# Kernel tuning notes

Hardware: AMD Instinct MI355X
Metric: run time of the kernel (lower is better)

The kernel has to match this reference:

```python
import jax, jax.numpy as jnp
import numpy as np

V, BLK, D, H, L = 50257, 2048, 768, 12, 4
HD = D // H
EPS = 1e-5


def _ln(x, w, b):
    mu = jnp.mean(x, axis=-1, keepdims=True)
    var = jnp.mean(jnp.square(x - mu), axis=-1, keepdims=True)
    return (x - mu) * jax.lax.rsqrt(var + EPS) * w + b


def setup_inputs() -> dict:
    key = jax.random.key(0)
    ks = iter(jax.random.split(key, 32))
    s = 0.02
    idx = jax.random.randint(next(ks), (2, 2048), 0, V)
    inp = {
        "idx": idx,
        "wte": jax.random.normal(next(ks), (V, D), jnp.float32) * s,
        "wpe": jax.random.normal(next(ks), (BLK, D), jnp.float32) * s,
        # stacked per-layer params [L, ...]
        "ln1_w": jnp.ones((L, D), jnp.float32),
        "ln1_b": jnp.zeros((L, D), jnp.float32),
        "attn_w": jax.random.normal(next(ks), (L, D, 3 * D), jnp.float32) * s,
        "attn_b": jnp.zeros((L, 3 * D), jnp.float32),
        "proj_w": jax.random.normal(next(ks), (L, D, D), jnp.float32) * (s / np.sqrt(2 * L)),
        "proj_b": jnp.zeros((L, D), jnp.float32),
        "ln2_w": jnp.ones((L, D), jnp.float32),
        "ln2_b": jnp.zeros((L, D), jnp.float32),
        "fc_w": jax.random.normal(next(ks), (L, D, 4 * D), jnp.float32) * s,
        "fc_b": jnp.zeros((L, 4 * D), jnp.float32),
        "fcp_w": jax.random.normal(next(ks), (L, 4 * D, D), jnp.float32) * (s / np.sqrt(2 * L)),
        "fcp_b": jnp.zeros((L, D), jnp.float32),
        "lnf_w": jnp.ones((D,), jnp.float32),
        "lnf_b": jnp.zeros((D,), jnp.float32),
    }
    return inp


def _gpt_forward(idx, wte, wpe, ln1_w, ln1_b, attn_w, attn_b, proj_w, proj_b,
                 ln2_w, ln2_b, fc_w, fc_b, fcp_w, fcp_b, lnf_w, lnf_b):
    B, T = idx.shape
    x = wte[idx] + wpe[:T]  # [B,T,D]; dropout p=0 -> identity
    causal = jnp.tril(jnp.ones((T, T), bool))
    scale = 1.0 / np.sqrt(HD)

    def block(x, p):
        l1w, l1b, aw, ab, pw, pb, l2w, l2b, fw, fb, fpw, fpb = p
        h = _ln(x, l1w, l1b)
        qkv = h @ aw + ab  # [B,T,3D]
        q, k, v = jnp.split(qkv, 3, axis=-1)
        q = q.reshape(B, T, H, HD).transpose(0, 2, 1, 3)  # [B,H,T,hd]
        k = k.reshape(B, T, H, HD).transpose(0, 2, 1, 3)
        v = v.reshape(B, T, H, HD).transpose(0, 2, 1, 3)
        att = jnp.einsum('bhqd,bhkd->bhqk', q, k) * scale
        att = jnp.where(causal, att, -jnp.inf)
        att = jax.nn.softmax(att, axis=-1)
        y = jnp.einsum('bhqk,bhkd->bhqd', att, v)
        y = y.transpose(0, 2, 1, 3).reshape(B, T, D)
        x = x + y @ pw + pb
        h2 = _ln(x, l2w, l2b)
        m = jax.nn.gelu(h2 @ fw + fb, approximate=False) @ fpw + fpb
        return x + m, None

    params = (ln1_w, ln1_b, attn_w, attn_b, proj_w, proj_b,
              ln2_w, ln2_b, fc_w, fc_b, fcp_w, fcp_b)
    x, _ = jax.lax.scan(block, x, params)
    x = _ln(x, lnf_w, lnf_b)
    # inference path: logits only for last position, lm_head tied to wte
    logits = x[:, -1:, :] @ wte.T  # [B,1,V]
    return logits


def reference(idx, wte, wpe, ln1_w, ln1_b, attn_w, attn_b, proj_w, proj_b,
              ln2_w, ln2_b, fc_w, fc_b, fcp_w, fcp_b, lnf_w, lnf_b):
    return _gpt_forward(idx, wte, wpe, ln1_w, ln1_b, attn_w, attn_b, proj_w, proj_b,
                        ln2_w, ln2_b, fc_w, fc_b, fcp_w, fcp_b, lnf_w, lnf_b)
```

## Files before the change

kernel.cpp:

```cpp
#include <hip/hip_runtime.h>
#include <math.h>

#define V 50257
#define B 2
#define T 2048
#define D 768
#define H 12
#define HD 64
#define L 4
#define D3 (3*D)
#define D4 (4*D)
#define NTOK (B*T)
#define EPS 1e-5f

typedef __bf16 v8bf __attribute__((ext_vector_type(8)));
typedef __bf16 v4bf __attribute__((ext_vector_type(4)));
typedef unsigned short v8us __attribute__((ext_vector_type(8)));
typedef float  v4f  __attribute__((ext_vector_type(4)));

#define GAS(p) ((const __attribute__((address_space(1))) void*)(p))
#define LAS(p) ((__attribute__((address_space(3))) void*)(p))

#define LIDX(row, chunk) ((row)*64 + ((((chunk) ^ ((row)&7)))<<3))

__global__ __launch_bounds__(256) void embed_kernel(const int* __restrict__ idx,
                                                    const float* __restrict__ wte,
                                                    const float* __restrict__ wpe,
                                                    float* __restrict__ x) {
    int i = blockIdx.x * 256 + threadIdx.x;
    if (i >= NTOK * D) return;
    int pos = i / D;
    int d   = i - pos * D;
    int t   = pos & (T - 1);
    int tok = idx[pos];
    x[i] = wte[tok * D + d] + wpe[t * D + d];
}

__global__ __launch_bounds__(256) void ln_kernel(const float* __restrict__ X,
                                                 const float* __restrict__ w,
                                                 const float* __restrict__ b,
                                                 __bf16* __restrict__ Y,
                                                 int src_mul, int src_off) {
    int srow = blockIdx.x * src_mul + src_off;
    const float* xr = X + (size_t)srow * D;
    float v[3];
    float s = 0.f, s2 = 0.f;
    #pragma unroll
    for (int j = 0; j < 3; ++j) {
        v[j] = xr[threadIdx.x + 256 * j];
        s += v[j];
        s2 += v[j] * v[j];
    }
    #pragma unroll
    for (int off = 32; off; off >>= 1) {
        s  += __shfl_xor(s, off);
        s2 += __shfl_xor(s2, off);
    }
    __shared__ float ss[4], ss2[4];
    int wave = threadIdx.x >> 6, lane = threadIdx.x & 63;
    if (lane == 0) { ss[wave] = s; ss2[wave] = s2; }
    __syncthreads();
    s  = ss[0] + ss[1] + ss[2] + ss[3];
    s2 = ss2[0] + ss2[1] + ss2[2] + ss2[3];
    float mu  = s * (1.f / D);
    float var = s2 * (1.f / D) - mu * mu;
    float rs  = rsqrtf(var + EPS);
    __bf16* yr = Y + (size_t)blockIdx.x * D;
    #pragma unroll
    for (int j = 0; j < 3; ++j) {
        int c = threadIdx.x + 256 * j;
        yr[c] = (__bf16)((v[j] - mu) * rs * w[c] + b[c]);
    }
}

__global__ __launch_bounds__(256) void convw4_kernel(
        const float* __restrict__ aw_all,  const float* __restrict__ pw_all,
        const float* __restrict__ fw_all,  const float* __restrict__ fpw_all,
        __bf16* __restrict__ awt_all, __bf16* __restrict__ pwt_all,
        __bf16* __restrict__ fwt_all, __bf16* __restrict__ fpwt_all) {
    int bid = blockIdx.x;
    const int l = bid / 6912; bid -= l * 6912;
    const float* W; __bf16* Wt; int K, N, bx, by;
    if (bid < 1728)      {             W = aw_all  + (size_t)l * D  * D3; Wt = awt_all  + (size_t)l * D3 * D;  K = D;  N = D3; bx = bid % 72; by = bid / 72; }
    else if (bid < 2304) { bid -= 1728; W = pw_all  + (size_t)l * D  * D;  Wt = pwt_all  + (size_t)l * D  * D;  K = D;  N = D;  bx = bid % 24; by = bid / 24; }
    else if (bid < 4608) { bid -= 2304; W = fw_all  + (size_t)l * D  * D4; Wt = fwt_all  + (size_t)l * D4 * D;  K = D;  N = D4; bx = bid % 96; by = bid / 96; }
    else                 { bid -= 4608; W = fpw_all + (size_t)l * D4 * D;  Wt = fpwt_all + (size_t)l * D  * D4; K = D4; N = D;  bx = bid % 24; by = bid / 24; }
    __shared__ float t[32][33];
    const int n0 = bx * 32, k0 = by * 32;
    const int tx = threadIdx.x & 31, ty = threadIdx.x >> 5;
    #pragma unroll
    for (int p = 0; p < 4; ++p)
        t[ty + 8 * p][tx] = W[(size_t)(k0 + ty + 8 * p) * N + n0 + tx];
    __syncthreads();
    #pragma unroll
    for (int p = 0; p < 4; ++p)
        Wt[(size_t)(n0 + ty + 8 * p) * K + k0 + tx] = (__bf16)t[tx][ty + 8 * p];
}

template<bool OUTBF16, bool DOGELU, bool DORES>
__global__ __launch_bounds__(256) void gemm_bt(const __bf16* __restrict__ A,
                                               const __bf16* __restrict__ Wt,
                                               const float* __restrict__ bias,
                                               const float* __restrict__ res,
                                               void* __restrict__ Cout,
                                               int N, int K) {
    __shared__ __align__(16) __bf16 As[4096];
    __shared__ __align__(16) __bf16 Bs[4096];
    const int tid  = threadIdx.x;
    const int w    = tid >> 6;
    const int lane = tid & 63;
    const int row0 = blockIdx.y * 128;
    const int col0 = blockIdx.x * 128;

    const int c0   = w * 64 + lane;
    const int srow = ((c0 >> 6) & 3) * 16 + (c0 & 15);
    const int sk   = ((c0 >> 4) & 3) * 8;
    const __bf16* gA0 = A  + (size_t)(row0 + srow) * K + sk;
    const __bf16* gA1 = gA0 + (size_t)64 * K;
    const __bf16* gB0 = Wt + (size_t)(col0 + srow) * K + sk;
    const __bf16* gB1 = gB0 + (size_t)64 * K;
    __bf16* lA0 = As + (size_t)c0 * 8;
    __bf16* lA1 = As + (size_t)(c0 + 256) * 8;
    __bf16* lB0 = Bs + (size_t)c0 * 8;
    __bf16* lB1 = Bs + (size_t)(c0 + 256) * 8;

    const int wr = w >> 1, wc = w & 1;
    const __bf16* rA = As + wr * 2048 + lane * 8;
    const __bf16* rB = Bs + wc * 2048 + lane * 8;

    v4f acc[4][4] = {};
    for (int k0 = 0; k0 < K; k0 += 32) {
        __builtin_amdgcn_global_load_lds(GAS(gA0), LAS(lA0), 16, 0, 0);
        __builtin_amdgcn_global_load_lds(GAS(gA1), LAS(lA1), 16, 0, 0);
        __builtin_amdgcn_global_load_lds(GAS(gB0), LAS(lB0), 16, 0, 0);
        __builtin_amdgcn_global_load_lds(GAS(gB1), LAS(lB1), 16, 0, 0);
        gA0 += 32; gA1 += 32; gB0 += 32; gB1 += 32;
        __syncthreads();
        v8bf af[4], bfr[4];
        #pragma unroll
        for (int i = 0; i < 4; ++i) af[i]  = *(const v8bf*)(rA + i * 512);
        #pragma unroll
        for (int j = 0; j < 4; ++j) bfr[j] = *(const v8bf*)(rB + j * 512);
        #pragma unroll
        for (int i = 0; i < 4; ++i)
            #pragma unroll
            for (int j = 0; j < 4; ++j)
                acc[i][j] = __builtin_amdgcn_mfma_f32_16x16x32_bf16(af[i], bfr[j], acc[i][j], 0, 0, 0);
        __syncthreads();
    }

    const int er = (lane >> 4) * 4;
    const int ec = lane & 15;
    #pragma unroll
    for (int j = 0; j < 4; ++j) {
        const int col = col0 + wc * 64 + j * 16 + ec;
        const float bval = bias[col];
        #pragma unroll
        for (int i = 0; i < 4; ++i) {
            #pragma unroll
            for (int rr = 0; rr < 4; ++rr) {
                const int row = row0 + wr * 64 + i * 16 + er + rr;
                float vv = acc[i][j][rr] + bval;
                if (DOGELU) vv = 0.5f * vv * (1.f + erff(vv * 0.70710678118f));
                if (DORES)  vv += res[(size_t)row * N + col];
                if (OUTBF16) ((__bf16*)Cout)[(size_t)row * N + col] = (__bf16)vv;
                else         ((float*) Cout)[(size_t)row * N + col] = vv;
            }
        }
    }
}

template<bool OUTBF16, bool DOGELU, bool DORES>
__global__ __launch_bounds__(256) void gemm_bt64(const __bf16* __restrict__ A,
                                                 const __bf16* __restrict__ Wt,
                                                 const float* __restrict__ bias,
                                                 const float* __restrict__ res,
                                                 void* __restrict__ Cout,
                                                 int N, int K) {
    __shared__ __align__(16) __bf16 As[4096];
    __shared__ __align__(16) __bf16 Bs[2048];
    const int tid  = threadIdx.x;
    const int w    = tid >> 6;
    const int lane = tid & 63;
    const int row0 = blockIdx.y * 128;
    const int col0 = blockIdx.x * 64;

    const int c0   = w * 64 + lane;
    const int srow = ((c0 >> 6) & 3) * 16 + (c0 & 15);
    const int sk   = ((c0 >> 4) & 3) * 8;
    const __bf16* gA0 = A  + (size_t)(row0 + srow) * K + sk;
    const __bf16* gA1 = gA0 + (size_t)64 * K;
    const __bf16* gB0 = Wt + (size_t)(col0 + srow) * K + sk;
    __bf16* lA0 = As + (size_t)c0 * 8;
    __bf16* lA1 = As + (size_t)(c0 + 256) * 8;
    __bf16* lB0 = Bs + (size_t)c0 * 8;

    const int wr = w >> 1, wc = w & 1;
    const __bf16* rA = As + wr * 2048 + lane * 8;
    const __bf16* rB = Bs + wc * 1024 + lane * 8;

    v4f acc[4][2] = {};
    for (int k0 = 0; k0 < K; k0 += 32) {
        __builtin_amdgcn_global_load_lds(GAS(gA0), LAS(lA0), 16, 0, 0);
        __builtin_amdgcn_global_load_lds(GAS(gA1), LAS(lA1), 16, 0, 0);
        __builtin_amdgcn_global_load_lds(GAS(gB0), LAS(lB0), 16, 0, 0);
        gA0 += 32; gA1 += 32; gB0 += 32;
        __syncthreads();
        v8bf af[4], bfr[2];
        #pragma unroll
        for (int i = 0; i < 4; ++i) af[i]  = *(const v8bf*)(rA + i * 512);
        #pragma unroll
        for (int j = 0; j < 2; ++j) bfr[j] = *(const v8bf*)(rB + j * 512);
        #pragma unroll
        for (int i = 0; i < 4; ++i)
            #pragma unroll
            for (int j = 0; j < 2; ++j)
                acc[i][j] = __builtin_amdgcn_mfma_f32_16x16x32_bf16(af[i], bfr[j], acc[i][j], 0, 0, 0);
        __syncthreads();
    }

    const int er = (lane >> 4) * 4;
    const int ec = lane & 15;
    #pragma unroll
    for (int j = 0; j < 2; ++j) {
        const int col = col0 + wc * 32 + j * 16 + ec;
        const float bval = bias[col];
        #pragma unroll
        for (int i = 0; i < 4; ++i) {
            #pragma unroll
            for (int rr = 0; rr < 4; ++rr) {
                const int row = row0 + wr * 64 + i * 16 + er + rr;
                float vv = acc[i][j][rr] + bval;
                if (DOGELU) vv = 0.5f * vv * (1.f + erff(vv * 0.70710678118f));
                if (DORES)  vv += res[(size_t)row * N + col];
                if (OUTBF16) ((__bf16*)Cout)[(size_t)row * N + col] = (__bf16)vv;
                else         ((float*) Cout)[(size_t)row * N + col] = vv;
            }
        }
    }
}

__global__ __launch_bounds__(256) void attn_mfma(const __bf16* __restrict__ qkv,
                                                 __bf16* __restrict__ y) {
    __shared__ __align__(16) __bf16 Qs[4096];
    __shared__ __align__(16) __bf16 Ks[4096];
    __shared__ __align__(16) __bf16 Vt[4096];
    __shared__ __align__(16) __bf16 Ps[4][1024];

    const int tid  = threadIdx.x;
    const int w    = tid >> 6;
    const int lane = tid & 63;
    const int quad = lane >> 4;
    const int l4   = lane & 15;

    const int qt = 31 - (blockIdx.x & 31);
    const int bh = blockIdx.x >> 5;
    const int b  = bh / H;
    const int h  = bh - b * H;
    const int q0 = qt * 64;

    const __bf16* base = qkv + (size_t)(b * T) * D3 + h * HD;

    {
        int c = tid;
        #pragma unroll
        for (int rep = 0; rep < 2; ++rep, c += 256) {
            int row = c >> 3, ch = c & 7;
            v8us v = *(const v8us*)(const void*)(base + (size_t)(q0 + row) * D3 + ch * 8);
            *(v8us*)(void*)(Qs + LIDX(row, ch)) = v;
        }
    }

    const int krow = tid >> 3, kch = tid & 7;
    const int vkp = tid & 31, vdc = tid >> 5;
    const __bf16* kp0 = base + D     + (size_t)krow * D3 + kch * 8;
    const __bf16* kp1 = kp0 + (size_t)32 * D3;
    const __bf16* vp0 = base + 2 * D + (size_t)(2 * vkp) * D3 + vdc * 8;
    const __bf16* vp1 = vp0 + D3;

    v8us kr0 = *(const v8us*)(const void*)kp0;
    v8us kr1 = *(const v8us*)(const void*)kp1;
    v8us vr0 = *(const v8us*)(const void*)vp0;
    v8us vr1 = *(const v8us*)(const void*)vp1;

    float m_local = -INFINITY;
    v4f o[4] = {};
    v4f sacc = {};
    v8bf qf[2];
    v8bf vones;
    #pragma unroll
    for (int i = 0; i < 8; ++i) vones[i] = (__bf16)1.0f;

    const int nt = qt + 1;
    const size_t adv = (size_t)64 * D3;
    const int qrow = q0 + w * 16 + l4;

    for (int kt = 0; kt < nt; ++kt) {
        const int k0 = kt * 64;
        *(v8us*)(void*)(Ks + LIDX(krow, kch))      = kr0;
        *(v8us*)(void*)(Ks + LIDX(krow + 32, kch)) = kr1;
        #pragma unroll
        for (int j = 0; j < 8; ++j) {
            int dim = vdc * 8 + j;
            int idx = dim * 64 + ((((vkp >> 2) ^ (dim & 7))) << 3) + ((vkp & 3) << 1);
            *(unsigned int*)(void*)(Vt + idx) =
                ((unsigned int)vr1[j] << 16) | (unsigned int)vr0[j];
        }
        __syncthreads();

        if (kt == 0) {
            #pragma unroll
            for (int kh = 0; kh < 2; ++kh)
                qf[kh] = *(const v8bf*)(Qs + LIDX(w * 16 + l4, kh * 4 + quad));
        }
        if (kt + 1 < nt) {
            kp0 += adv; kp1 += adv; vp0 += adv; vp1 += adv;
            kr0 = *(const v8us*)(const void*)kp0;
            kr1 = *(const v8us*)(const void*)kp1;
            vr0 = *(const v8us*)(const void*)vp0;
            vr1 = *(const v8us*)(const void*)vp1;
        }

        v4f s[4] = {};
        __builtin_amdgcn_s_setprio(1);
        #pragma unroll
        for (int kh = 0; kh < 2; ++kh) {
            #pragma unroll
            for (int jb = 0; jb < 4; ++jb) {
                v8bf bk = *(const v8bf*)(Ks + LIDX(jb * 16 + l4, kh * 4 + quad));
                s[jb] = __builtin_amdgcn_mfma_f32_16x16x32_bf16(bk, qf[kh], s[jb], 0, 0, 0);
            }
        }
        __builtin_amdgcn_s_setprio(0);

        float sv[4][4];
        float mx = -INFINITY;
        #pragma unroll
        for (int jb = 0; jb < 4; ++jb) {
            #pragma unroll
            for (int rg = 0; rg < 4; ++rg) {
                float vvv = s[jb][rg] * 0.125f;
                if (k0 + jb * 16 + quad * 4 + rg > qrow) vvv = -INFINITY;
                sv[jb][rg] = vvv;
                mx = fmaxf(mx, vvv);
            }
        }
        mx = fmaxf(mx, __shfl_xor(mx, 16));
        mx = fmaxf(mx, __shfl_xor(mx, 32));
        const float mnew   = fmaxf(m_local, mx);
        const float alpha_l = __expf(m_local - mnew);
        m_local = mnew;
        #pragma unroll
        for (int jb = 0; jb < 4; ++jb) {
            v4bf pk;
            #pragma unroll
            for (int rg = 0; rg < 4; ++rg)
                pk[rg] = (__bf16)__expf(sv[jb][rg] - mnew);
            *(v4bf*)(void*)(&Ps[w][LIDX(l4, jb * 2 + (quad >> 1)) + ((quad & 1) << 2)]) = pk;
        }
        float a4[4];
        #pragma unroll
        for (int r = 0; r < 4; ++r) a4[r] = __shfl(alpha_l, quad * 4 + r);
        #pragma unroll
        for (int r = 0; r < 4; ++r) {
            sacc[r] *= a4[r];
            #pragma unroll
            for (int db = 0; db < 4; ++db) o[db][r] *= a4[r];
        }
        __builtin_amdgcn_s_setprio(1);
        #pragma unroll
        for (int kh = 0; kh < 2; ++kh) {
            v8bf ap = *(const v8bf*)(&Ps[w][LIDX(l4, kh * 4 + quad)]);
            sacc = __builtin_amdgcn_mfma_f32_16x16x32_bf16(ap, vones, sacc, 0, 0, 0);
            #pragma unroll
            for (int db = 0; db < 4; ++db) {
                v8bf bv = *(const v8bf*)(Vt + LIDX(db * 16 + l4, kh * 4 + quad));
                o[db] = __builtin_amdgcn_mfma_f32_16x16x32_bf16(ap, bv, o[db], 0, 0, 0);
            }
        }
        __builtin_amdgcn_s_setprio(0);
        __syncthreads();
    }

    #pragma unroll
    for (int db = 0; db < 4; ++db) {
        #pragma unroll
        for (int r = 0; r < 4; ++r) {
            const int q = q0 + w * 16 + quad * 4 + r;
            y[(size_t)(b * T + q) * D + h * HD + db * 16 + l4] =
                (__bf16)(o[db][r] / sacc[r]);
        }
    }
}

__global__ __launch_bounds__(256) void logits_kernel(const __bf16* __restrict__ xf,
                                                     const float* __restrict__ wte,
                                                     float* __restrict__ out) {
    int wave = threadIdx.x >> 6;
    int lane = threadIdx.x & 63;
    int gid = blockIdx.x * 4 + wave;
    if (gid >= B * V) return;
    int b = gid / V;
    int v = gid - b * V;
    const float* wr = wte + (size_t)v * D;
    const __bf16* xr = xf + b * D;
    float s = 0.f;
    #pragma unroll
    for (int j = 0; j < 12; ++j)
        s = fmaf(wr[lane + 64 * j], (float)xr[lane + 64 * j], s);
    #pragma unroll
    for (int off = 32; off; off >>= 1) s += __shfl_xor(s, off);
    if (lane == 0) out[gid] = s;
}

extern "C" void kernel_launch(void* const* d_in, const int* in_sizes, int n_in,
                              void* d_out, int out_size, void* d_ws, size_t ws_size,
                              hipStream_t stream) {
    const int*   idx    = (const int*)  d_in[0];
    const float* wte    = (const float*)d_in[1];
    const float* wpe    = (const float*)d_in[2];
    const float* ln1_w  = (const float*)d_in[3];
    const float* ln1_b  = (const float*)d_in[4];
    const float* attn_w = (const float*)d_in[5];
    const float* attn_b = (const float*)d_in[6];
    const float* proj_w = (const float*)d_in[7];
    const float* proj_b = (const float*)d_in[8];
    const float* ln2_w  = (const float*)d_in[9];
    const float* ln2_b  = (const float*)d_in[10];
    const float* fc_w   = (const float*)d_in[11];
    const float* fc_b   = (const float*)d_in[12];
    const float* fcp_w  = (const float*)d_in[13];
    const float* fcp_b  = (const float*)d_in[14];
    const float* lnf_w  = (const float*)d_in[15];
    const float* lnf_b  = (const float*)d_in[16];
    float* out = (float*)d_out;

    char* ws = (char*)d_ws;
    float*  x    = (float*)ws;  ws += (size_t)NTOK * D  * 4;
    __bf16* qkvb = (__bf16*)ws;
    __bf16* gb   = (__bf16*)ws; ws += (size_t)NTOK * D4 * 2;
    __bf16* hb   = (__bf16*)ws; ws += (size_t)NTOK * D  * 2;
    __bf16* yb   = (__bf16*)ws; ws += (size_t)NTOK * D  * 2;
    __bf16* awt  = (__bf16*)ws; ws += (size_t)L * D3 * D   * 2;
    __bf16* pwt  = (__bf16*)ws; ws += (size_t)L * D  * D   * 2;
    __bf16* fwt  = (__bf16*)ws; ws += (size_t)L * D4 * D   * 2;
    __bf16* fpwt = (__bf16*)ws; ws += (size_t)L * D  * D4  * 2;
    __bf16* xf   = (__bf16*)ws; ws += (size_t)B * D    * 2;

    embed_kernel<<<(NTOK * D + 255) / 256, 256, 0, stream>>>(idx, wte, wpe, x);

    convw4_kernel<<<6912 * L, 256, 0, stream>>>(attn_w, proj_w, fc_w, fcp_w,
                                                awt, pwt, fwt, fpwt);

    for (int l = 0; l < L; ++l) {
        const float* l1w = ln1_w + l * D;
        const float* l1b = ln1_b + l * D;
        const float* ab  = attn_b + l * D3;
        const float* pb  = proj_b + l * D;
        const float* l2w = ln2_w + l * D;
        const float* l2b = ln2_b + l * D;
        const float* fb  = fc_b + l * D4;
        const float* fpb = fcp_b + l * D;
        const __bf16* awl  = awt  + (size_t)l * D3 * D;
        const __bf16* pwl  = pwt  + (size_t)l * D  * D;
        const __bf16* fwl  = fwt  + (size_t)l * D4 * D;
        const __bf16* fpwl = fpwt + (size_t)l * D  * D4;

        ln_kernel<<<NTOK, 256, 0, stream>>>(x, l1w, l1b, hb, 1, 0);
        gemm_bt<true, false, false><<<dim3(D3 / 128, NTOK / 128), 256, 0, stream>>>(
            hb, awl, ab, nullptr, qkvb, D3, D);
        attn_mfma<<<B * H * (T / 64), 256, 0, stream>>>(qkvb, yb);
        gemm_bt64<false, false, true><<<dim3(D / 64, NTOK / 128), 256, 0, stream>>>(
            yb, pwl, pb, x, x, D, D);
        ln_kernel<<<NTOK, 256, 0, stream>>>(x, l2w, l2b, hb, 1, 0);
        gemm_bt<true, true, false><<<dim3(D4 / 128, NTOK / 128), 256, 0, stream>>>(
            hb, fwl, fb, nullptr, gb, D4, D);
        gemm_bt64<false, false, true><<<dim3(D / 64, NTOK / 128), 256, 0, stream>>>(
            gb, fpwl, fpb, x, x, D, D4);
    }

    ln_kernel<<<B, 256, 0, stream>>>(x, lnf_w, lnf_b, xf, T, T - 1);
    logits_kernel<<<(B * V + 3) / 4, 256, 0, stream>>>(xf, wte, out);
}
```

Baseline: 1.367 ms.

## Fuse prep kernels, deepen GEMM K-tile, lazy softmax rescale, batch logits

```diff
diff --git a/kernel.cpp b/kernel.cpp
--- a/kernel.cpp
+++ b/kernel.cpp
@@ -23,17 +23,43 @@
 
 #define LIDX(row, chunk) ((row)*64 + ((((chunk) ^ ((row)&7)))<<3))
 
-__global__ __launch_bounds__(256) void embed_kernel(const int* __restrict__ idx,
-                                                    const float* __restrict__ wte,
-                                                    const float* __restrict__ wpe,
-                                                    float* __restrict__ x) {
-    int i = blockIdx.x * 256 + threadIdx.x;
-    if (i >= NTOK * D) return;
-    int pos = i / D;
-    int d   = i - pos * D;
-    int t   = pos & (T - 1);
-    int tok = idx[pos];
-    x[i] = wte[tok * D + d] + wpe[t * D + d];
+__global__ __launch_bounds__(256) void prep_kernel(
+        const int* __restrict__ idx, const float* __restrict__ wte,
+        const float* __restrict__ wpe, float* __restrict__ x,
+        const float* __restrict__ aw_all,  const float* __restrict__ pw_all,
+        const float* __restrict__ fw_all,  const float* __restrict__ fpw_all,
+        __bf16* __restrict__ awt_all, __bf16* __restrict__ pwt_all,
+        __bf16* __restrict__ fwt_all, __bf16* __restrict__ fpwt_all) {
+    int bid = blockIdx.x;
+    if (bid < 3072) {
+        int e = (bid * 256 + threadIdx.x) * 4;
+        int pos = e / D;
+        int d   = e - pos * D;
+        int t   = pos & (T - 1);
+        int tok = idx[pos];
+        const float4 a  = *(const float4*)(wte + (size_t)tok * D + d);
+        const float4 p4 = *(const float4*)(wpe + (size_t)t * D + d);
+        float4 r; r.x = a.x + p4.x; r.y = a.y + p4.y; r.z = a.z + p4.z; r.w = a.w + p4.w;
+        *(float4*)(x + e) = r;
+        return;
+    }
+    bid -= 3072;
+    const int l = bid / 6912; bid -= l * 6912;
+    const float* W; __bf16* Wt; int K, N, bx, by;
+    if (bid < 1728)      {             W = aw_all  + (size_t)l * D  * D3; Wt = awt_all  + (size_t)l * D3 * D;  K = D;  N = D3; bx = bid % 72; by = bid / 72; }
+    else if (bid < 2304) { bid -= 1728; W = pw_all  + (size_t)l * D  * D;  Wt = pwt_all  + (size_t)l * D  * D;  K = D;  N = D;  bx = bid % 24; by = bid / 24; }
+    else if (bid < 4608) { bid -= 2304; W = fw_all  + (size_t)l * D  * D4; Wt = fwt_all  + (size_t)l * D4 * D;  K = D;  N = D4; bx = bid % 96; by = bid / 96; }
+    else                 { bid -= 4608; W = fpw_all + (size_t)l * D4 * D;  Wt = fpwt_all + (size_t)l * D  * D4; K = D4; N = D;  bx = bid % 24; by = bid / 24; }
+    __shared__ float t[32][33];
+    const int n0 = bx * 32, k0 = by * 32;
+    const int tx = threadIdx.x & 31, ty = threadIdx.x >> 5;
+    #pragma unroll
+    for (int p = 0; p < 4; ++p)
+        t[ty + 8 * p][tx] = W[(size_t)(k0 + ty + 8 * p) * N + n0 + tx];
+    __syncthreads();
+    #pragma unroll
+    for (int p = 0; p < 4; ++p)
+        Wt[(size_t)(n0 + ty + 8 * p) * K + k0 + tx] = (__bf16)t[tx][ty + 8 * p];
 }
 
 __global__ __launch_bounds__(256) void ln_kernel(const float* __restrict__ X,
@@ -73,30 +99,6 @@
     }
 }
 
-__global__ __launch_bounds__(256) void convw4_kernel(
-        const float* __restrict__ aw_all,  const float* __restrict__ pw_all,
-        const float* __restrict__ fw_all,  const float* __restrict__ fpw_all,
-        __bf16* __restrict__ awt_all, __bf16* __restrict__ pwt_all,
-        __bf16* __restrict__ fwt_all, __bf16* __restrict__ fpwt_all) {
-    int bid = blockIdx.x;
-    const int l = bid / 6912; bid -= l * 6912;
-    const float* W; __bf16* Wt; int K, N, bx, by;
-    if (bid < 1728)      {             W = aw_all  + (size_t)l * D  * D3; Wt = awt_all  + (size_t)l * D3 * D;  K = D;  N = D3; bx = bid % 72; by = bid / 72; }
-    else if (bid < 2304) { bid -= 1728; W = pw_all  + (size_t)l * D  * D;  Wt = pwt_all  + (size_t)l * D  * D;  K = D;  N = D;  bx = bid % 24; by = bid / 24; }
-    else if (bid < 4608) { bid -= 2304; W = fw_all  + (size_t)l * D  * D4; Wt = fwt_all  + (size_t)l * D4 * D;  K = D;  N = D4; bx = bid % 96; by = bid / 96; }
-    else                 { bid -= 4608; W = fpw_all + (size_t)l * D4 * D;  Wt = fpwt_all + (size_t)l * D  * D4; K = D4; N = D;  bx = bid % 24; by = bid / 24; }
-    __shared__ float t[32][33];
-    const int n0 = bx * 32, k0 = by * 32;
-    const int tx = threadIdx.x & 31, ty = threadIdx.x >> 5;
-    #pragma unroll
-    for (int p = 0; p < 4; ++p)
-        t[ty + 8 * p][tx] = W[(size_t)(k0 + ty + 8 * p) * N + n0 + tx];
-    __syncthreads();
-    #pragma unroll
-    for (int p = 0; p < 4; ++p)
-        Wt[(size_t)(n0 + ty + 8 * p) * K + k0 + tx] = (__bf16)t[tx][ty + 8 * p];
-}
-
 template<bool OUTBF16, bool DOGELU, bool DORES>
 __global__ __launch_bounds__(256) void gemm_bt(const __bf16* __restrict__ A,
                                                const __bf16* __restrict__ Wt,
@@ -104,15 +106,15 @@
                                                const float* __restrict__ res,
                                                void* __restrict__ Cout,
                                                int N, int K) {
-    __shared__ __align__(16) __bf16 As[4096];
-    __shared__ __align__(16) __bf16 Bs[4096];
+    __shared__ __align__(16) __bf16 As[8192];
+    __shared__ __align__(16) __bf16 Bs[8192];
     const int tid  = threadIdx.x;
     const int w    = tid >> 6;
     const int lane = tid & 63;
     const int row0 = blockIdx.y * 128;
     const int col0 = blockIdx.x * 128;
 
-    const int c0   = w * 64 + lane;
+    const int c0   = tid;
     const int srow = ((c0 >> 6) & 3) * 16 + (c0 & 15);
     const int sk   = ((c0 >> 4) & 3) * 8;
     const __bf16* gA0 = A  + (size_t)(row0 + srow) * K + sk;
@@ -121,31 +123,42 @@
     const __bf16* gB1 = gB0 + (size_t)64 * K;
     __bf16* lA0 = As + (size_t)c0 * 8;
     __bf16* lA1 = As + (size_t)(c0 + 256) * 8;
+    __bf16* lA2 = As + 4096 + (size_t)c0 * 8;
+    __bf16* lA3 = As + 4096 + (size_t)(c0 + 256) * 8;
     __bf16* lB0 = Bs + (size_t)c0 * 8;
     __bf16* lB1 = Bs + (size_t)(c0 + 256) * 8;
+    __bf16* lB2 = Bs + 4096 + (size_t)c0 * 8;
+    __bf16* lB3 = Bs + 4096 + (size_t)(c0 + 256) * 8;
 
     const int wr = w >> 1, wc = w & 1;
     const __bf16* rA = As + wr * 2048 + lane * 8;
     const __bf16* rB = Bs + wc * 2048 + lane * 8;
 
     v4f acc[4][4] = {};
-    for (int k0 = 0; k0 < K; k0 += 32) {
-        __builtin_amdgcn_global_load_lds(GAS(gA0), LAS(lA0), 16, 0, 0);
-        __builtin_amdgcn_global_load_lds(GAS(gA1), LAS(lA1), 16, 0, 0);
-        __builtin_amdgcn_global_load_lds(GAS(gB0), LAS(lB0), 16, 0, 0);
-        __builtin_amdgcn_global_load_lds(GAS(gB1), LAS(lB1), 16, 0, 0);
-        gA0 += 32; gA1 += 32; gB0 += 32; gB1 += 32;
+    for (int k0 = 0; k0 < K; k0 += 64) {
+        __builtin_amdgcn_global_load_lds(GAS(gA0),      LAS(lA0), 16, 0, 0);
+        __builtin_amdgcn_global_load_lds(GAS(gA1),      LAS(lA1), 16, 0, 0);
+        __builtin_amdgcn_global_load_lds(GAS(gA0 + 32), LAS(lA2), 16, 0, 0);
+        __builtin_amdgcn_global_load_lds(GAS(gA1 + 32), LAS(lA3), 16, 0, 0);
+        __builtin_amdgcn_global_load_lds(GAS(gB0),      LAS(lB0), 16, 0, 0);
+        __builtin_amdgcn_global_load_lds(GAS(gB1),      LAS(lB1), 16, 0, 0);
+        __builtin_amdgcn_global_load_lds(GAS(gB0 + 32), LAS(lB2), 16, 0, 0);
+        __builtin_amdgcn_global_load_lds(GAS(gB1 + 32), LAS(lB3), 16, 0, 0);
+        gA0 += 64; gA1 += 64; gB0 += 64; gB1 += 64;
         __syncthreads();
-        v8bf af[4], bfr[4];
-        #pragma unroll
-        for (int i = 0; i < 4; ++i) af[i]  = *(const v8bf*)(rA + i * 512);
-        #pragma unroll
-        for (int j = 0; j < 4; ++j) bfr[j] = *(const v8bf*)(rB + j * 512);
-        #pragma unroll
-        for (int i = 0; i < 4; ++i)
-            #pragma unroll
-            for (int j = 0; j < 4; ++j)
-                acc[i][j] = __builtin_amdgcn_mfma_f32_16x16x32_bf16(af[i], bfr[j], acc[i][j], 0, 0, 0);
+        #pragma unroll
+        for (int h = 0; h < 2; ++h) {
+            v8bf af[4], bfr[4];
+            #pragma unroll
+            for (int i = 0; i < 4; ++i) af[i]  = *(const v8bf*)(rA + h * 4096 + i * 512);
+            #pragma unroll
+            for (int j = 0; j < 4; ++j) bfr[j] = *(const v8bf*)(rB + h * 4096 + j * 512);
+            #pragma unroll
+            for (int i = 0; i < 4; ++i)
+                #pragma unroll
+                for (int j = 0; j < 4; ++j)
+                    acc[i][j] = __builtin_amdgcn_mfma_f32_16x16x32_bf16(af[i], bfr[j], acc[i][j], 0, 0, 0);
+        }
         __syncthreads();
     }
 
@@ -177,15 +190,15 @@
                                                  const float* __restrict__ res,
                                                  void* __restrict__ Cout,
                                                  int N, int K) {
-    __shared__ __align__(16) __bf16 As[4096];
-    __shared__ __align__(16) __bf16 Bs[2048];
+    __shared__ __align__(16) __bf16 As[8192];
+    __shared__ __align__(16) __bf16 Bs[4096];
     const int tid  = threadIdx.x;
     const int w    = tid >> 6;
     const int lane = tid & 63;
     const int row0 = blockIdx.y * 128;
     const int col0 = blockIdx.x * 64;
 
-    const int c0   = w * 64 + lane;
+    const int c0   = tid;
     const int srow = ((c0 >> 6) & 3) * 16 + (c0 & 15);
     const int sk   = ((c0 >> 4) & 3) * 8;
     const __bf16* gA0 = A  + (size_t)(row0 + srow) * K + sk;
@@ -193,29 +206,38 @@
     const __bf16* gB0 = Wt + (size_t)(col0 + srow) * K + sk;
     __bf16* lA0 = As + (size_t)c0 * 8;
     __bf16* lA1 = As + (size_t)(c0 + 256) * 8;
+    __bf16* lA2 = As + 4096 + (size_t)c0 * 8;
+    __bf16* lA3 = As + 4096 + (size_t)(c0 + 256) * 8;
     __bf16* lB0 = Bs + (size_t)c0 * 8;
+    __bf16* lB1 = Bs + 2048 + (size_t)c0 * 8;
 
     const int wr = w >> 1, wc = w & 1;
     const __bf16* rA = As + wr * 2048 + lane * 8;
     const __bf16* rB = Bs + wc * 1024 + lane * 8;
 
     v4f acc[4][2] = {};
-    for (int k0 = 0; k0 < K; k0 += 32) {
-        __builtin_amdgcn_global_load_lds(GAS(gA0), LAS(lA0), 16, 0, 0);
-        __builtin_amdgcn_global_load_lds(GAS(gA1), LAS(lA1), 16, 0, 0);
-        __builtin_amdgcn_global_load_lds(GAS(gB0), LAS(lB0), 16, 0, 0);
-        gA0 += 32; gA1 += 32; gB0 += 32;
+    for (int k0 = 0; k0 < K; k0 += 64) {
+        __builtin_amdgcn_global_load_lds(GAS(gA0),      LAS(lA0), 16, 0, 0);
+        __builtin_amdgcn_global_load_lds(GAS(gA1),      LAS(lA1), 16, 0, 0);
+        __builtin_amdgcn_global_load_lds(GAS(gA0 + 32), LAS(lA2), 16, 0, 0);
+        __builtin_amdgcn_global_load_lds(GAS(gA1 + 32), LAS(lA3), 16, 0, 0);
+        __builtin_amdgcn_global_load_lds(GAS(gB0),      LAS(lB0), 16, 0, 0);
+        __builtin_amdgcn_global_load_lds(GAS(gB0 + 32), LAS(lB1), 16, 0, 0);
+        gA0 += 64; gA1 += 64; gB0 += 64;
         __syncthreads();
-        v8bf af[4], bfr[2];
-        #pragma unroll
-        for (int i = 0; i < 4; ++i) af[i]  = *(const v8bf*)(rA + i * 512);
-        #pragma unroll
-        for (int j = 0; j < 2; ++j) bfr[j] = *(const v8bf*)(rB + j * 512);
-        #pragma unroll
-        for (int i = 0; i < 4; ++i)
-            #pragma unroll
-            for (int j = 0; j < 2; ++j)
-                acc[i][j] = __builtin_amdgcn_mfma_f32_16x16x32_bf16(af[i], bfr[j], acc[i][j], 0, 0, 0);
+        #pragma unroll
+        for (int h = 0; h < 2; ++h) {
+            v8bf af[4], bfr[2];
+            #pragma unroll
+            for (int i = 0; i < 4; ++i) af[i]  = *(const v8bf*)(rA + h * 4096 + i * 512);
+            #pragma unroll
+            for (int j = 0; j < 2; ++j) bfr[j] = *(const v8bf*)(rB + h * 2048 + j * 512);
+            #pragma unroll
+            for (int i = 0; i < 4; ++i)
+                #pragma unroll
+                for (int j = 0; j < 2; ++j)
+                    acc[i][j] = __builtin_amdgcn_mfma_f32_16x16x32_bf16(af[i], bfr[j], acc[i][j], 0, 0, 0);
+        }
         __syncthreads();
     }
 
@@ -347,25 +369,27 @@
         }
         mx = fmaxf(mx, __shfl_xor(mx, 16));
         mx = fmaxf(mx, __shfl_xor(mx, 32));
-        const float mnew   = fmaxf(m_local, mx);
-        const float alpha_l = __expf(m_local - mnew);
-        m_local = mnew;
+        if (!__all(mx <= m_local + 8.f)) {
+            const float mnew    = fmaxf(m_local, mx);
+            const float alpha_l = __expf(m_local - mnew);
+            m_local = mnew;
+            float a4[4];
+            #pragma unroll
+            for (int r = 0; r < 4; ++r) a4[r] = __shfl(alpha_l, quad * 4 + r);
+            #pragma unroll
+            for (int r = 0; r < 4; ++r) {
+                sacc[r] *= a4[r];
+                #pragma unroll
+                for (int db = 0; db < 4; ++db) o[db][r] *= a4[r];
+            }
+        }
         #pragma unroll
         for (int jb = 0; jb < 4; ++jb) {
             v4bf pk;
             #pragma unroll
             for (int rg = 0; rg < 4; ++rg)
-                pk[rg] = (__bf16)__expf(sv[jb][rg] - mnew);
+                pk[rg] = (__bf16)__expf(sv[jb][rg] - m_local);
             *(v4bf*)(void*)(&Ps[w][LIDX(l4, jb * 2 + (quad >> 1)) + ((quad & 1) << 2)]) = pk;
-        }
-        float a4[4];
-        #pragma unroll
-        for (int r = 0; r < 4; ++r) a4[r] = __shfl(alpha_l, quad * 4 + r);
-        #pragma unroll
-        for (int r = 0; r < 4; ++r) {
-            sacc[r] *= a4[r];
-            #pragma unroll
-            for (int db = 0; db < 4; ++db) o[db][r] *= a4[r];
         }
         __builtin_amdgcn_s_setprio(1);
         #pragma unroll
@@ -398,19 +422,28 @@
                                                      float* __restrict__ out) {
     int wave = threadIdx.x >> 6;
     int lane = threadIdx.x & 63;
-    int gid = blockIdx.x * 4 + wave;
-    if (gid >= B * V) return;
-    int b = gid / V;
-    int v = gid - b * V;
-    const float* wr = wte + (size_t)v * D;
-    const __bf16* xr = xf + b * D;
-    float s = 0.f;
-    #pragma unroll
-    for (int j = 0; j < 12; ++j)
-        s = fmaf(wr[lane + 64 * j], (float)xr[lane + 64 * j], s);
-    #pragma unroll
-    for (int off = 32; off; off >>= 1) s += __shfl_xor(s, off);
-    if (lane == 0) out[gid] = s;
+    int v = blockIdx.x * 4 + wave;
+    if (v >= V) return;
+    const float4* wr = (const float4*)(wte + (size_t)v * D);
+    const v4bf*   x0 = (const v4bf*)(xf);
+    const v4bf*   x1 = (const v4bf*)(xf + D);
+    float s0 = 0.f, s1 = 0.f;
+    #pragma unroll
+    for (int j = 0; j < 3; ++j) {
+        float4 wv = wr[lane + 64 * j];
+        v4bf a0 = x0[lane + 64 * j];
+        v4bf a1 = x1[lane + 64 * j];
+        s0 = fmaf(wv.x, (float)a0[0], s0); s0 = fmaf(wv.y, (float)a0[1], s0);
+        s0 = fmaf(wv.z, (float)a0[2], s0); s0 = fmaf(wv.w, (float)a0[3], s0);
+        s1 = fmaf(wv.x, (float)a1[0], s1); s1 = fmaf(wv.y, (float)a1[1], s1);
+        s1 = fmaf(wv.z, (float)a1[2], s1); s1 = fmaf(wv.w, (float)a1[3], s1);
+    }
+    #pragma unroll
+    for (int off = 32; off; off >>= 1) {
+        s0 += __shfl_xor(s0, off);
+        s1 += __shfl_xor(s1, off);
+    }
+    if (lane == 0) { out[v] = s0; out[V + v] = s1; }
 }
 
 extern "C" void kernel_launch(void* const* d_in, const int* in_sizes, int n_in,
@@ -447,10 +480,9 @@
     __bf16* fpwt = (__bf16*)ws; ws += (size_t)L * D  * D4  * 2;
     __bf16* xf   = (__bf16*)ws; ws += (size_t)B * D    * 2;
 
-    embed_kernel<<<(NTOK * D + 255) / 256, 256, 0, stream>>>(idx, wte, wpe, x);
-
-    convw4_kernel<<<6912 * L, 256, 0, stream>>>(attn_w, proj_w, fc_w, fcp_w,
-                                                awt, pwt, fwt, fpwt);
+    prep_kernel<<<3072 + 6912 * L, 256, 0, stream>>>(idx, wte, wpe, x,
+                                                     attn_w, proj_w, fc_w, fcp_w,
+                                                     awt, pwt, fwt, fpwt);
 
     for (int l = 0; l < L; ++l) {
         const float* l1w = ln1_w + l * D;
@@ -480,5 +512,5 @@
     }
 
     ln_kernel<<<B, 256, 0, stream>>>(x, lnf_w, lnf_b, xf, T, T - 1);
-    logits_kernel<<<(B * V + 3) / 4, 256, 0, stream>>>(xf, wte, out);
-}
+    logits_kernel<<<(V + 3) / 4, 256, 0, stream>>>(xf, wte, out);
+}
```

Result: faster. 1.334 ms (-2.4%).
